# Performance work log

Measured on AMD Instinct MI355X. Metric: run time of the kernel, lower is better.

## Reference

```python
import jax, jax.numpy as jnp
import numpy as np

D_MODEL = 1024
NUM_HEADS = 16
D_HEAD = D_MODEL // NUM_HEADS
THETA = 10000.0
B, S = 2, 2048


def setup_inputs() -> dict:
    key = jax.random.key(0)
    ks = jax.random.split(key, 5)
    std = np.sqrt(2.0 / (D_MODEL + D_MODEL))
    x = jax.random.normal(ks[0], (B, S, D_MODEL), dtype=jnp.float32)
    Wq = jax.random.normal(ks[1], (D_MODEL, D_MODEL), dtype=jnp.float32) * std
    Wk = jax.random.normal(ks[2], (D_MODEL, D_MODEL), dtype=jnp.float32) * std
    Wv = jax.random.normal(ks[3], (D_MODEL, D_MODEL), dtype=jnp.float32) * std
    Wo = jax.random.normal(ks[4], (D_MODEL, D_MODEL), dtype=jnp.float32) * std
    token_positions = jnp.arange(S, dtype=jnp.int32)
    return {"x": x, "Wq": Wq, "Wk": Wk, "Wv": Wv, "Wo": Wo,
            "token_positions": token_positions}


def _apply_rope(t, token_positions):
    # t: [B, H, S, d_head]; interleaved (even/odd) RoPE
    dh = t.shape[-1]
    inv_freq = 1.0 / (THETA ** (jnp.arange(0, dh, 2, dtype=jnp.float32) / dh))
    freqs = token_positions.astype(jnp.float32)[:, None] * inv_freq  # [S, dh/2]
    cos = jnp.cos(freqs)  # broadcasts over B, H
    sin = jnp.sin(freqs)
    x1 = t[..., 0::2]
    x2 = t[..., 1::2]
    r1 = x1 * cos - x2 * sin
    r2 = x1 * sin + x2 * cos
    return jnp.stack([r1, r2], axis=-1).reshape(t.shape)


def reference(x, Wq, Wk, Wv, Wo, token_positions):
    b, s, d = x.shape
    h, dh = NUM_HEADS, D_HEAD

    def proj(W):
        y = x @ W.T  # [B, S, D]
        return y.reshape(b, s, h, dh).transpose(0, 2, 1, 3)  # [B, H, S, dh]

    q = _apply_rope(proj(Wq), token_positions)
    k = _apply_rope(proj(Wk), token_positions)
    v = proj(Wv)

    scores = jnp.einsum('bhqd,bhkd->bhqk', q, k) / jnp.sqrt(jnp.float32(dh))
    causal = jnp.tril(jnp.ones((s, s), dtype=bool))
    scores = jnp.where(causal, scores, jnp.float32(-jnp.inf))
    attn = jax.nn.softmax(scores, axis=-1)
    out = jnp.einsum('bhqk,bhkd->bhqd', attn, v)  # [B, H, S, dh]
    out = out.transpose(0, 2, 1, 3).reshape(b, s, d)
    return out @ Wo.T
```

## Files before the change

### kernel.cpp

```cpp
#include <hip/hip_runtime.h>
#include <hip/hip_bf16.h>
#include <math.h>

#define DMODEL 1024
#define NHEAD  16
#define DHEAD  64
#define BATCH  2
#define SEQ    2048
#define MROWS  (BATCH * SEQ)

typedef __attribute__((ext_vector_type(8))) __bf16 bf16x8;
typedef __attribute__((ext_vector_type(4))) float  f32x4;

__device__ __forceinline__ void load16_lds(const ushort* g, ushort* l) {
    __builtin_amdgcn_global_load_lds(
        (const __attribute__((address_space(1))) unsigned int*)g,
        (__attribute__((address_space(3))) unsigned int*)l, 16, 0, 0);
}

__device__ __forceinline__ ushort bf16u(float v) {
    __hip_bfloat16 h = __float2bfloat16(v);
    return *reinterpret_cast<ushort*>(&h);
}

__global__ __launch_bounds__(256)
void cast_f32_bf16(const float* __restrict__ s, ushort* __restrict__ d, int n) {
    const int i = (blockIdx.x * 256 + threadIdx.x) * 8;
    if (i >= n) return;
    const f32x4 a = *reinterpret_cast<const f32x4*>(s + i);
    const f32x4 b = *reinterpret_cast<const f32x4*>(s + i + 4);
    bf16x8 o;
    #pragma unroll
    for (int j = 0; j < 4; j++) { o[j] = (__bf16)a[j]; o[4 + j] = (__bf16)b[j]; }
    *reinterpret_cast<bf16x8*>(d + i) = o;
}

__global__ __launch_bounds__(256)
void cast_w4(const float* __restrict__ w0, const float* __restrict__ w1,
             const float* __restrict__ w2, const float* __restrict__ w3,
             ushort* __restrict__ dst) {
    const float* src = (blockIdx.y == 0) ? w0 : (blockIdx.y == 1) ? w1
                     : (blockIdx.y == 2) ? w2 : w3;
    const int i = (blockIdx.x * 256 + threadIdx.x) * 8;
    const f32x4 a = *reinterpret_cast<const f32x4*>(src + i);
    const f32x4 b = *reinterpret_cast<const f32x4*>(src + i + 4);
    bf16x8 o;
    #pragma unroll
    for (int j = 0; j < 4; j++) { o[j] = (__bf16)a[j]; o[4 + j] = (__bf16)b[j]; }
    *reinterpret_cast<bf16x8*>(dst + (size_t)blockIdx.y * DMODEL * DMODEL + i) = o;
}

__global__ __launch_bounds__(256)
void rope_tab(const int* __restrict__ pos, float2* __restrict__ tab) {
    const int idx = blockIdx.x * 256 + threadIdx.x;
    const int s = idx >> 5;
    const int i = idx & 31;
    const float p = (float)pos[s];
    const float inv = exp2f(-(float)i * 0.41524101186092f);
    float sn, cs;
    sincosf(p * inv, &sn, &cs);
    tab[idx] = make_float2(cs, sn);
}

#define QKV_BARRIER() do { asm volatile("" ::: "memory"); \
                           __builtin_amdgcn_s_barrier(); } while (0)

#define PH_READ_AB(KS)                                                        \
    {                                                                         \
        const ushort* pA_ = pool + buf + (KS) * 8192 + (wm + l16) * 32 + chq; \
        _Pragma("unroll")                                                     \
        for (int im = 0; im < 8; im++)                                        \
            af[im] = *reinterpret_cast<const bf16x8*>(pA_ + im * 512);        \
        const ushort* pB_ = pool + buf + 16384 + (KS) * 8192 +                \
                            (wn + l16) * 32 + chq;                            \
        _Pragma("unroll")                                                     \
        for (int jn = 0; jn < 4; jn++)                                        \
            bf[jn] = *reinterpret_cast<const bf16x8*>(pB_ + jn * 512);        \
    }

#define PH_MFMA2()                                                            \
    __builtin_amdgcn_s_setprio(1);                                            \
    _Pragma("unroll")                                                         \
    for (int im = 0; im < 8; im++)                                            \
        _Pragma("unroll")                                                     \
        for (int jn = 0; jn < 4; jn++)                                        \
            acc[im][jn] = __builtin_amdgcn_mfma_f32_16x16x32_bf16(            \
                af[im], bf[jn], acc[im][jn], 0, 0, 0);                        \
    __builtin_amdgcn_s_setprio(0);

__global__ __launch_bounds__(512, 2)
void gemm_qkv(const ushort* __restrict__ A, const ushort* __restrict__ B,
              ushort* __restrict__ C, const float2* __restrict__ tab) {
    __shared__ __align__(16) ushort pool[65536];

    const int orig = blockIdx.y * gridDim.x + blockIdx.x;
    const int xcd  = orig & 7;
    const int ixd  = orig >> 3;
    const int by   = xcd * 2 + (ixd / 12);
    const int bx   = ixd % 12;
    const int m0   = by * 256;
    const int n0   = bx * 256;

    const int tid  = threadIdx.x;
    const int lane = tid & 63;
    const int w    = tid >> 6;
    const int l16  = lane & 15;
    const int quad = lane >> 4;
    const int wm   = (w >> 2) * 128;
    const int wn   = (w & 3) * 64;
    const int chq  = (quad ^ ((l16 & 3) ^ ((l16 & 4) >> 1))) << 3;
    const int srow = tid >> 2;
    const int ssc  = (tid & 3) ^ ((srow & 3) ^ ((srow & 4) >> 1));

    const ushort* gA = A + (size_t)(m0 + srow) * DMODEL + ssc * 8;
    const ushort* gB = B + (size_t)(n0 + srow) * DMODEL + ssc * 8;

    auto stageA = [&](int tt, int ks) {
        const int off = tt * 64 + ks * 32;
        const int lb  = ((tt & 1) << 15) + (ks << 13);
        load16_lds(gA + off,               &pool[lb + tid * 8]);
        load16_lds(gA + 128 * DMODEL + off, &pool[lb + 4096 + tid * 8]);
    };
    auto stageB = [&](int tt, int ks) {
        const int off = tt * 64 + ks * 32;
        const int lb  = ((tt & 1) << 15) + 16384 + (ks << 13);
        load16_lds(gB + off,               &pool[lb + tid * 8]);
        load16_lds(gB + 128 * DMODEL + off, &pool[lb + 4096 + tid * 8]);
    };

    stageA(0, 0); stageB(0, 0);
    stageA(0, 1); stageB(0, 1);
    stageA(1, 0); stageB(1, 0);

    f32x4 acc[8][4];
    #pragma unroll
    for (int i = 0; i < 8; i++)
        #pragma unroll
        for (int j = 0; j < 4; j++) acc[i][j] = (f32x4){0.f, 0.f, 0.f, 0.f};

    asm volatile("s_waitcnt vmcnt(8)" ::: "memory");
    __builtin_amdgcn_s_barrier();

    bf16x8 af[8], bf[4];

    #pragma unroll 1
    for (int t = 0; t < 16; t++) {
        const int buf = (t & 1) << 15;
        PH_READ_AB(0);
        if (t <= 14) { stageA(t + 1, 1); stageB(t + 1, 1); }
        QKV_BARRIER();
        PH_MFMA2();
        if (t <= 14) { asm volatile("s_waitcnt vmcnt(8)" ::: "memory"); }
        else         { asm volatile("s_waitcnt vmcnt(0)" ::: "memory"); }
        QKV_BARRIER();
        PH_READ_AB(1);
        if (t <= 13) { stageA(t + 2, 0); stageB(t + 2, 0); }
        QKV_BARRIER();
        PH_MFMA2();
        if (t <= 13)      { asm volatile("s_waitcnt vmcnt(8)" ::: "memory"); }
        else if (t == 14) { asm volatile("s_waitcnt vmcnt(4)" ::: "memory"); }
        QKV_BARRIER();
    }

    const int nbase  = n0 + wn;
    const int tensor = nbase >> 10;
    const int hh     = (nbase & 1023) >> 6;
    if (tensor < 2) {
        ushort* Dt = C + (size_t)tensor * ((size_t)MROWS * DMODEL);
        #pragma unroll
        for (int i = 0; i < 8; i++)
            #pragma unroll
            for (int r = 0; r < 4; r++) {
                const int m  = m0 + wm + i * 16 + quad * 4 + r;
                const int bb = m >> 11;
                const int ss = m & (SEQ - 1);
                const float2* trow = tab + ss * 32;
                #pragma unroll
                for (int j = 0; j < 4; j++) {
                    const int f = j * 16 + l16;
                    const float2 cs = trow[f >> 1];
                    const float val = acc[i][j][r];
                    const float prt = __shfl_xor(val, 1, 64);
                    const float out = (f & 1) ? (prt * cs.y + val * cs.x)
                                              : (val * cs.x - prt * cs.y);
                    Dt[(((size_t)(bb * NHEAD + hh)) * SEQ + ss) * DHEAD + f] =
                        bf16u(out);
                }
            }
    } else {
        ushort* Tw = pool + w * 8192;
        #pragma unroll
        for (int i = 0; i < 8; i++)
            #pragma unroll
            for (int j = 0; j < 4; j++) {
                const int f  = j * 16 + l16;
                const int sx = (f & 7) << 3;
                #pragma unroll
                for (int r = 0; r < 4; r += 2) {
                    const int ml = i * 16 + quad * 4 + r;
                    ushort2 pk;
                    pk.x = bf16u(acc[i][j][r]);
                    pk.y = bf16u(acc[i][j][r + 1]);
                    *reinterpret_cast<ushort2*>(&Tw[f * 128 + (ml ^ sx)]) = pk;
                }
            }
        asm volatile("s_waitcnt lgkmcnt(0)" ::: "memory");
        ushort* Dv = C + 2 * ((size_t)MROWS * DMODEL);
        const int c  = lane & 15;
        const int fb = lane >> 4;
        #pragma unroll
        for (int rr = 0; rr < 16; rr++) {
            const int fl = rr * 4 + fb;
            const uint4 v = *reinterpret_cast<const uint4*>(
                &Tw[fl * 128 + ((c << 3) ^ ((fl & 7) << 3))]);
            *reinterpret_cast<uint4*>(
                &Dv[(size_t)(hh * 64 + fl) * MROWS + m0 + wm + (c << 3)]) = v;
        }
    }
}

__global__ __launch_bounds__(256)
void gemm_out64(const ushort* __restrict__ A, const ushort* __restrict__ B,
                float* __restrict__ C) {
    __shared__ __align__(16) ushort pool[12288];
    ushort* As = pool;
    ushort* Bs = pool + 4096;
    const int tid  = threadIdx.x;
    const int m0   = blockIdx.y * 64;
    const int n0   = blockIdx.x * 128;
    const int lane = tid & 63;
    const int w    = tid >> 6;
    const int l16  = lane & 15;
    const int quad = lane >> 4;
    const int wm   = (w >> 1) * 32;
    const int wn   = (w & 1) * 64;
    const int srow = tid >> 2;
    const int scol = (tid & 3) * 8;

    const int am  = m0 + srow;
    const int abb = am >> 11;
    const int ass = am & (SEQ - 1);
    const size_t abase = ((size_t)(abb * NHEAD)) * SEQ * DHEAD + (size_t)ass * DHEAD;

    f32x4 acc[2][4];
    #pragma unroll
    for (int i = 0; i < 2; i++)
        #pragma unroll
        for (int j = 0; j < 4; j++) acc[i][j] = (f32x4){0.f, 0.f, 0.f, 0.f};

    {
        const int h = scol >> 6, dh = scol & 63;
        load16_lds(A + abase + (size_t)h * SEQ * DHEAD + dh, &As[srow * 32 + scol]);
        #pragma unroll
        for (int half = 0; half < 2; half++) {
            const int row = srow + half * 64;
            load16_lds(B + (size_t)(n0 + row) * DMODEL + scol, &Bs[row * 32 + scol]);
        }
    }

    for (int t = 0; t < 32; t++) {
        const int bf = t & 1;
        __syncthreads();
        if (t + 1 < 32) {
            const int k0 = (t + 1) * 32;
            const int kk = k0 + scol;
            const int h = kk >> 6, dh = kk & 63;
            load16_lds(A + abase + (size_t)h * SEQ * DHEAD + dh,
                       &As[(bf ^ 1) * 2048 + srow * 32 + scol]);
            #pragma unroll
            for (int half = 0; half < 2; half++) {
                const int row = srow + half * 64;
                load16_lds(B + (size_t)(n0 + row) * DMODEL + k0 + scol,
                           &Bs[(bf ^ 1) * 4096 + row * 32 + scol]);
            }
        }
        const int oa = bf * 2048, ob_ = bf * 4096;
        bf16x8 af[2], bfr[4];
        #pragma unroll
        for (int s = 0; s < 2; s++)
            af[s] = *reinterpret_cast<const bf16x8*>(
                &As[oa + (wm + s * 16 + l16) * 32 + quad * 8]);
        #pragma unroll
        for (int s = 0; s < 4; s++)
            bfr[s] = *reinterpret_cast<const bf16x8*>(
                &Bs[ob_ + (wn + s * 16 + l16) * 32 + quad * 8]);
        #pragma unroll
        for (int i = 0; i < 2; i++)
            #pragma unroll
            for (int j = 0; j < 4; j++)
                acc[i][j] = __builtin_amdgcn_mfma_f32_16x16x32_bf16(
                    af[i], bfr[j], acc[i][j], 0, 0, 0);
    }
    #pragma unroll
    for (int i = 0; i < 2; i++)
        #pragma unroll
        for (int r = 0; r < 4; r++) {
            const int m = m0 + wm + i * 16 + quad * 4 + r;
            #pragma unroll
            for (int j = 0; j < 4; j++)
                C[(size_t)m * DMODEL + n0 + wn + j * 16 + l16] = acc[i][j][r];
        }
}

__global__ __launch_bounds__(256)
void attn_mfma6(const ushort* __restrict__ qb, const ushort* __restrict__ kb,
                const ushort* __restrict__ vtg, ushort* __restrict__ ob) {
    __shared__ __align__(16) ushort Ks[2][4096];
    __shared__ __align__(16) ushort Vs[2][4096];
    __shared__ ushort Pb[4][16][72];

    const int bh   = blockIdx.x;
    const int b    = bh >> 4;
    const int h    = bh & 15;
    const int qt   = (gridDim.y - 1) - blockIdx.y;
    const int tid  = threadIdx.x;
    const int w    = tid >> 6;
    const int lane = tid & 63;
    const int l16  = lane & 15;
    const int quad = lane >> 4;
    const size_t base = (size_t)bh * SEQ * DHEAD;

    const int qlo = qt * 64 + w * 16;

    const float SC = 0.125f * 1.44269504088896f;
    bf16x8 qa[2];
    {
        const size_t qo = base + (size_t)(qlo + l16) * DHEAD + quad * 8;
        qa[0] = *reinterpret_cast<const bf16x8*>(qb + qo);
        qa[1] = *reinterpret_cast<const bf16x8*>(qb + qo + 32);
        #pragma unroll
        for (int j = 0; j < 8; j++) {
            qa[0][j] = (__bf16)(SC * (float)qa[0][j]);
            qa[1][j] = (__bf16)(SC * (float)qa[1][j]);
        }
    }

    f32x4 oacc[4];
    #pragma unroll
    for (int s = 0; s < 4; s++) oacc[s] = (f32x4){0.f, 0.f, 0.f, 0.f};
    float l_ = 0.f;

    const int c0 = tid,        r0 = c0 >> 3, g0 = (c0 & 7) ^ (r0 & 7);
    const int c1 = 256 + tid,  r1 = c1 >> 3, g1 = (c1 & 7) ^ (r1 & 7);
    const ushort* kg0 = kb + base + (size_t)r0 * DHEAD + g0 * 8;
    const ushort* kg1 = kb + base + (size_t)r1 * DHEAD + g1 * 8;
    const ushort* vg0 = vtg + (size_t)(h * DHEAD + r0) * MROWS + b * SEQ + g0 * 8;
    const ushort* vg1 = vtg + (size_t)(h * DHEAD + r1) * MROWS + b * SEQ + g1 * 8;

    int koff[2][4];
    #pragma unroll
    for (int half = 0; half < 2; half++)
        #pragma unroll
        for (int sub = 0; sub < 4; sub++)
            koff[half][sub] = (sub * 16 + l16) * 64 +
                              (((half * 4 + quad) ^ (l16 & 7)) * 8);

    load16_lds(kg0, &Ks[0][c0 * 8]);
    load16_lds(kg1, &Ks[0][c1 * 8]);
    load16_lds(vg0, &Vs[0][c0 * 8]);
    load16_lds(vg1, &Vs[0][c1 * 8]);

    const int T = qt + 1;
    for (int t = 0; t < T; t++) {
        const int bf = t & 1;
        __syncthreads();
        if (t + 1 < T) {
            const size_t ko = (size_t)(t + 1) * 64 * DHEAD;
            const int    vo = (t + 1) * 64;
            load16_lds(kg0 + ko, &Ks[bf ^ 1][c0 * 8]);
            load16_lds(kg1 + ko, &Ks[bf ^ 1][c1 * 8]);
            load16_lds(vg0 + vo, &Vs[bf ^ 1][c0 * 8]);
            load16_lds(vg1 + vo, &Vs[bf ^ 1][c1 * 8]);
        }

        const bool diag = (t == qt);
        const int nsub = diag ? (w + 1) : 4;
        const int nhv  = diag ? ((w >> 1) + 1) : 2;

        f32x4 sacc[4];
        #pragma unroll
        for (int s = 0; s < 4; s++) sacc[s] = (f32x4){0.f, 0.f, 0.f, 0.f};
        #pragma unroll
        for (int half = 0; half < 2; half++)
            #pragma unroll
            for (int sub = 0; sub < 4; sub++)
                if (sub < nsub) {
                    const bf16x8 kf = *reinterpret_cast<const bf16x8*>(
                        &Ks[bf][koff[half][sub]]);
                    sacc[sub] = __builtin_amdgcn_mfma_f32_16x16x32_bf16(
                        kf, qa[half], sacc[sub], 0, 0, 0);
                }

        float ev[4][4];
        if (diag) {
            const int thr = qlo + l16 - t * 64;
            #pragma unroll
            for (int sub = 0; sub < 4; sub++)
                #pragma unroll
                for (int r = 0; r < 4; r++) {
                    const float e = (sub * 16 + quad * 4 + r <= thr)
                                        ? exp2f(sacc[sub][r]) : 0.f;
                    ev[sub][r] = e;
                    l_ += e;
                }
        } else {
            #pragma unroll
            for (int sub = 0; sub < 4; sub++)
                #pragma unroll
                for (int r = 0; r < 4; r++) {
                    const float e = exp2f(sacc[sub][r]);
                    ev[sub][r] = e;
                    l_ += e;
                }
        }

        #pragma unroll
        for (int sub = 0; sub < 4; sub++) {
            ushort4 pk;
            pk.x = bf16u(ev[sub][0]); pk.y = bf16u(ev[sub][1]);
            pk.z = bf16u(ev[sub][2]); pk.w = bf16u(ev[sub][3]);
            *reinterpret_cast<ushort4*>(&Pb[w][l16][sub * 16 + quad * 4]) = pk;
        }
        bf16x8 pa[2];
        pa[0] = *reinterpret_cast<const bf16x8*>(&Pb[w][l16][quad * 8]);
        pa[1] = *reinterpret_cast<const bf16x8*>(&Pb[w][l16][32 + quad * 8]);

        #pragma unroll
        for (int hk = 0; hk < 2; hk++) {
            if (hk >= nhv) break;
            #pragma unroll
            for (int sf = 0; sf < 4; sf++) {
                const bf16x8 vf = *reinterpret_cast<const bf16x8*>(
                    &Vs[bf][koff[hk][sf]]);
                oacc[sf] = __builtin_amdgcn_mfma_f32_16x16x32_bf16(
                    pa[hk], vf, oacc[sf], 0, 0, 0);
            }
        }
    }

    l_ += __shfl_xor(l_, 16, 64);
    l_ += __shfl_xor(l_, 32, 64);
    float inv[4];
    #pragma unroll
    for (int r = 0; r < 4; r++) inv[r] = 1.f / __shfl(l_, quad * 4 + r, 64);
    #pragma unroll
    for (int sub = 0; sub < 4; sub++)
        #pragma unroll
        for (int r = 0; r < 4; r++) {
            const int q = qlo + quad * 4 + r;
            ob[base + (size_t)q * DHEAD + sub * 16 + l16] =
                bf16u(oacc[sub][r] * inv[r]);
        }
}

extern "C" void kernel_launch(void* const* d_in, const int* in_sizes, int n_in,
                              void* d_out, int out_size, void* d_ws, size_t ws_size,
                              hipStream_t stream) {
    const float* x  = (const float*)d_in[0];
    const float* Wq = (const float*)d_in[1];
    const float* Wk = (const float*)d_in[2];
    const float* Wv = (const float*)d_in[3];
    const float* Wo = (const float*)d_in[4];
    const int* pos = (const int*)d_in[5];

    const size_t TEN = (size_t)MROWS * DMODEL;
    const size_t WEL = (size_t)DMODEL * DMODEL;
    ushort* xb   = (ushort*)d_ws;
    ushort* Wqkv = xb + TEN;
    ushort* Wob  = Wqkv + 3 * WEL;
    ushort* qb   = Wob + WEL;
    ushort* kb   = qb + TEN;
    ushort* vtb  = kb + TEN;
    ushort* ob   = vtb + TEN;
    float2* tab  = (float2*)(ob + TEN);

    dim3 blk(256);
    rope_tab<<<(SEQ * 32) / 256, blk, 0, stream>>>(pos, tab);
    cast_f32_bf16<<<TEN / (8 * 256), blk, 0, stream>>>(x, xb, (int)TEN);
    dim3 gcw(WEL / (8 * 256), 4);
    cast_w4<<<gcw, blk, 0, stream>>>(Wq, Wk, Wv, Wo, Wqkv);

    dim3 gqkv(3 * DMODEL / 256, MROWS / 256);
    gemm_qkv<<<gqkv, dim3(512), 0, stream>>>(xb, Wqkv, qb, tab);

    dim3 gattn(BATCH * NHEAD, SEQ / 64);
    attn_mfma6<<<gattn, blk, 0, stream>>>(qb, kb, vtb, ob);

    dim3 gout(DMODEL / 128, MROWS / 64);
    gemm_out64<<<gout, blk, 0, stream>>>(ob, Wob, (float*)d_out);
}
```

Before: 184.8 us.

## Software-pipeline LDS fragment reads with MFMA in QKV GEMM main loop

```diff
diff --git a/kernel.cpp b/kernel.cpp
--- a/kernel.cpp
+++ b/kernel.cpp
@@ -65,27 +65,19 @@
 #define QKV_BARRIER() do { asm volatile("" ::: "memory"); \
                            __builtin_amdgcn_s_barrier(); } while (0)
 
-#define PH_READ_AB(KS)                                                        \
-    {                                                                         \
-        const ushort* pA_ = pool + buf + (KS) * 8192 + (wm + l16) * 32 + chq; \
-        _Pragma("unroll")                                                     \
-        for (int im = 0; im < 8; im++)                                        \
-            af[im] = *reinterpret_cast<const bf16x8*>(pA_ + im * 512);        \
-        const ushort* pB_ = pool + buf + 16384 + (KS) * 8192 +                \
-                            (wn + l16) * 32 + chq;                            \
-        _Pragma("unroll")                                                     \
-        for (int jn = 0; jn < 4; jn++)                                        \
-            bf[jn] = *reinterpret_cast<const bf16x8*>(pB_ + jn * 512);        \
-    }
-
-#define PH_MFMA2()                                                            \
+#define RD4(dst, p_)                                                          \
+    _Pragma("unroll")                                                         \
+    for (int rr_ = 0; rr_ < 4; rr_++)                                         \
+        dst[rr_] = *reinterpret_cast<const bf16x8*>((p_) + rr_ * 512);
+
+#define MFMA_G(AFR, BFR, IOFF)                                                \
     __builtin_amdgcn_s_setprio(1);                                            \
     _Pragma("unroll")                                                         \
-    for (int im = 0; im < 8; im++)                                            \
+    for (int im_ = 0; im_ < 4; im_++)                                         \
         _Pragma("unroll")                                                     \
-        for (int jn = 0; jn < 4; jn++)                                        \
-            acc[im][jn] = __builtin_amdgcn_mfma_f32_16x16x32_bf16(            \
-                af[im], bf[jn], acc[im][jn], 0, 0, 0);                        \
+        for (int jn_ = 0; jn_ < 4; jn_++)                                     \
+            acc[(IOFF) + im_][jn_] = __builtin_amdgcn_mfma_f32_16x16x32_bf16( \
+                AFR[im_], BFR[jn_], acc[(IOFF) + im_][jn_], 0, 0, 0);         \
     __builtin_amdgcn_s_setprio(0);
 
 __global__ __launch_bounds__(512, 2)
@@ -118,13 +110,13 @@
     auto stageA = [&](int tt, int ks) {
         const int off = tt * 64 + ks * 32;
         const int lb  = ((tt & 1) << 15) + (ks << 13);
-        load16_lds(gA + off,               &pool[lb + tid * 8]);
+        load16_lds(gA + off,                &pool[lb + tid * 8]);
         load16_lds(gA + 128 * DMODEL + off, &pool[lb + 4096 + tid * 8]);
     };
     auto stageB = [&](int tt, int ks) {
         const int off = tt * 64 + ks * 32;
         const int lb  = ((tt & 1) << 15) + 16384 + (ks << 13);
-        load16_lds(gB + off,               &pool[lb + tid * 8]);
+        load16_lds(gB + off,                &pool[lb + tid * 8]);
         load16_lds(gB + 128 * DMODEL + off, &pool[lb + 4096 + tid * 8]);
     };
 
@@ -138,27 +130,42 @@
         #pragma unroll
         for (int j = 0; j < 4; j++) acc[i][j] = (f32x4){0.f, 0.f, 0.f, 0.f};
 
-    asm volatile("s_waitcnt vmcnt(8)" ::: "memory");
+    asm volatile("s_waitcnt vmcnt(4)" ::: "memory");
     __builtin_amdgcn_s_barrier();
 
-    bf16x8 af[8], bf[4];
+    bf16x8 al[4], ah[4], bc[4], bn[4];
+
+    { const ushort* p = pool + (wm + l16) * 32 + chq;           RD4(al, p); }
+    { const ushort* q = pool + 16384 + (wn + l16) * 32 + chq;   RD4(bc, q); }
 
     #pragma unroll 1
     for (int t = 0; t < 16; t++) {
-        const int buf = (t & 1) << 15;
-        PH_READ_AB(0);
+        const int buf  = (t & 1) << 15;
+        const int bufn = buf ^ 32768;
         if (t <= 14) { stageA(t + 1, 1); stageB(t + 1, 1); }
+        { const ushort* p = pool + buf + (wm + 64 + l16) * 32 + chq;
+          RD4(ah, p); }
+        MFMA_G(al, bc, 0);
+        { const ushort* p = pool + buf + 8192 + (wm + l16) * 32 + chq;
+          RD4(al, p);
+          const ushort* q = pool + buf + 16384 + 8192 + (wn + l16) * 32 + chq;
+          RD4(bn, q); }
+        MFMA_G(ah, bc, 4);
+        if (t <= 14) { asm volatile("s_waitcnt vmcnt(4)" ::: "memory"); }
         QKV_BARRIER();
-        PH_MFMA2();
-        if (t <= 14) { asm volatile("s_waitcnt vmcnt(8)" ::: "memory"); }
-        else         { asm volatile("s_waitcnt vmcnt(0)" ::: "memory"); }
-        QKV_BARRIER();
-        PH_READ_AB(1);
         if (t <= 13) { stageA(t + 2, 0); stageB(t + 2, 0); }
-        QKV_BARRIER();
-        PH_MFMA2();
-        if (t <= 13)      { asm volatile("s_waitcnt vmcnt(8)" ::: "memory"); }
-        else if (t == 14) { asm volatile("s_waitcnt vmcnt(4)" ::: "memory"); }
+        { const ushort* p = pool + buf + 8192 + (wm + 64 + l16) * 32 + chq;
+          RD4(ah, p); }
+        MFMA_G(al, bn, 0);
+        if (t <= 14) {
+            const ushort* p = pool + bufn + (wm + l16) * 32 + chq;
+            RD4(al, p);
+            const ushort* q = pool + bufn + 16384 + (wn + l16) * 32 + chq;
+            RD4(bc, q);
+        }
+        MFMA_G(ah, bn, 4);
+        if (t <= 13)      { asm volatile("s_waitcnt vmcnt(4)" ::: "memory"); }
+        else if (t == 14) { asm volatile("s_waitcnt vmcnt(0)" ::: "memory"); }
         QKV_BARRIER();
     }
 
```

New measurement: 181.5 us. About the same (-1.8%).
